# Optimization experiments

Measured on AMD Instinct MI355X. Metric: run time of the kernel, lower is better.

## Reference

```python
import jax, jax.numpy as jnp
import numpy as np

H = 1024          # hiddenSize
V = 50257         # outputSize (vocab)
L = 512           # maxLength (encoder length)


def setup_inputs() -> dict:
    key = jax.random.key(0)
    ks = jax.random.split(key, 16)
    s = 0.02
    return {
        "input": jax.random.randint(ks[0], (1,), 0, V),
        "hidden": jax.random.normal(ks[1], (1, 1, H), jnp.float32),
        "encoder_outputs": jax.random.normal(ks[2], (L, H), jnp.float32),
        "emb": jax.random.normal(ks[3], (V, H), jnp.float32) * s,
        "W_attn": jax.random.normal(ks[4], (L, 2 * H), jnp.float32) * s,
        "b_attn": jnp.zeros((L,), jnp.float32),
        "W_comb": jax.random.normal(ks[5], (H, 2 * H), jnp.float32) * s,
        "b_comb": jnp.zeros((H,), jnp.float32),
        "W_ih": jax.random.normal(ks[6], (3 * H, H), jnp.float32) * s,
        "W_hh": jax.random.normal(ks[7], (3 * H, H), jnp.float32) * s,
        "b_ih": jnp.zeros((3 * H,), jnp.float32),
        "b_hh": jnp.zeros((3 * H,), jnp.float32),
        "W_out": jax.random.normal(ks[8], (V, H), jnp.float32) * s,
        "b_out": jnp.zeros((V,), jnp.float32),
    }


def reference(input, hidden, encoder_outputs, emb, W_attn, b_attn,
              W_comb, b_comb, W_ih, W_hh, b_ih, b_hh, W_out, b_out):
    # embedding lookup: [1, H] (dropout p=0 -> identity)
    embedded = emb[input]
    h = hidden[0]                                   # [1, H]
    # attention over encoder positions
    attn_logits = jnp.concatenate([embedded, h], axis=1) @ W_attn.T + b_attn
    attn_weights = jax.nn.softmax(attn_logits, axis=1)      # [1, L]
    attn_applied = attn_weights @ encoder_outputs           # [1, H]
    # combine and relu
    x = jnp.concatenate([embedded, attn_applied], axis=1) @ W_comb.T + b_comb
    x = jax.nn.relu(x)                                      # [1, H]
    # single GRU step (PyTorch gate layout: r, z, n)
    gi = x @ W_ih.T + b_ih                                  # [1, 3H]
    gh = h @ W_hh.T + b_hh                                  # [1, 3H]
    i_r, i_z, i_n = jnp.split(gi, 3, axis=1)
    h_r, h_z, h_n = jnp.split(gh, 3, axis=1)
    r = jax.nn.sigmoid(i_r + h_r)
    z = jax.nn.sigmoid(i_z + h_z)
    n = jnp.tanh(i_n + r * h_n)
    h_new = (1.0 - z) * n + z * h                           # [1, H]
    # output distribution
    output = jax.nn.log_softmax(h_new @ W_out.T + b_out, axis=1)  # [1, V]
    return output, h_new[None], attn_weights
```

## Files before the change

### kernel.cpp

```cpp
#include <hip/hip_runtime.h>
#include <cmath>

#define H 1024
#define V 50257
#define L 512
#define NB5 1571

__device__ __forceinline__ float wred_sum(float v) {
#pragma unroll
    for (int o = 32; o > 0; o >>= 1) v += __shfl_xor(v, o, 64);
    return v;
}
__device__ __forceinline__ float wred_max(float v) {
#pragma unroll
    for (int o = 32; o > 0; o >>= 1) v = fmaxf(v, __shfl_xor(v, o, 64));
    return v;
}
__device__ __forceinline__ float dot4(float4 a, float4 b) {
    return a.x * b.x + a.y * b.y + a.z * b.z + a.w * b.w;
}
__device__ __forceinline__ void ms_merge(float& m, float& s, float m2, float s2) {
    float M = fmaxf(m, m2);
    if (M == -INFINITY) { m = M; s = 0.f; return; }
    s = s * expf(m - M) + s2 * expf(m2 - M);
    m = M;
}

__global__ void k_phase1(const int* __restrict__ tok,
                         const float* __restrict__ hid,
                         const float* __restrict__ emb,
                         const float* __restrict__ Wa,
                         const float* __restrict__ ba,
                         const float* __restrict__ Whh,
                         const float* __restrict__ bhh,
                         float* __restrict__ lg,
                         float* __restrict__ gh,
                         float* __restrict__ aa) {
    const int t = threadIdx.x;
    const int lane = t & 63, wv = t >> 6;
    if (blockIdx.x < 512) {
        const int l = blockIdx.x;
        const float4* wr = (const float4*)(Wa + (size_t)l * 2048);
        const float4* e4 = (const float4*)(emb + (size_t)tok[0] * H);
        const float4* h4 = (const float4*)hid;
        float acc = 0.f;
#pragma unroll
        for (int i = 0; i < 2; ++i) {
            int f = t + i * 256;
            float4 w = wr[f];
            float4 s = (f < 256) ? e4[f] : h4[f - 256];
            acc += dot4(w, s);
        }
        __shared__ float sm[4];
        acc = wred_sum(acc);
        if (lane == 0) sm[wv] = acc;
        __syncthreads();
        if (t == 0) lg[l] = sm[0] + sm[1] + sm[2] + sm[3] + ba[l];
    } else {
        const int j = (blockIdx.x - 512) * 4 + wv;
        const float4* wh = (const float4*)(Whh + (size_t)j * H);
        const float4* h4 = (const float4*)hid;
        float acc = 0.f;
#pragma unroll
        for (int k = 0; k < 4; ++k) {
            int f = 64 * k + lane;
            acc += dot4(wh[f], h4[f]);
        }
        acc = wred_sum(acc);
        if (lane == 0) gh[j] = acc + bhh[j];
        if (blockIdx.x == 512) {
            aa[t] = 0.f; aa[t + 256] = 0.f; aa[t + 512] = 0.f; aa[t + 768] = 0.f;
        }
    }
}

__global__ void k_attn(const float* __restrict__ lg,
                       const float* __restrict__ enc,
                       float* __restrict__ wout,
                       float* __restrict__ aa) {
    const int t = threadIdx.x;
    const int lane = t & 63, wv = t >> 6;
    __shared__ float red[4];
    __shared__ float swL[512];
    float v0 = lg[t], v1 = lg[t + 256];
    float m = wred_max(fmaxf(v0, v1));
    if (lane == 0) red[wv] = m;
    __syncthreads();
    const float M = fmaxf(fmaxf(red[0], red[1]), fmaxf(red[2], red[3]));
    float e0 = expf(v0 - M), e1 = expf(v1 - M);
    float sl = wred_sum(e0 + e1);
    __syncthreads();
    if (lane == 0) red[wv] = sl;
    __syncthreads();
    const float S = red[0] + red[1] + red[2] + red[3];
    swL[t] = e0 / S;
    swL[t + 256] = e1 / S;
    __syncthreads();
    if (blockIdx.x == 0) { wout[t] = swL[t]; wout[t + 256] = swL[t + 256]; }
    const int l0 = blockIdx.x * 16;
    float a0 = 0.f, a1 = 0.f, a2 = 0.f, a3 = 0.f;
#pragma unroll 4
    for (int l = l0; l < l0 + 16; ++l) {
        const float w = swL[l];
        const float* er = enc + (size_t)l * H;
        a0 += w * er[t];
        a1 += w * er[t + 256];
        a2 += w * er[t + 512];
        a3 += w * er[t + 768];
    }
    atomicAdd(&aa[t], a0);
    atomicAdd(&aa[t + 256], a1);
    atomicAdd(&aa[t + 512], a2);
    atomicAdd(&aa[t + 768], a3);
}

__global__ void k_comb(const int* __restrict__ tok,
                       const float* __restrict__ emb,
                       const float* __restrict__ aa,
                       const float* __restrict__ Wc,
                       const float* __restrict__ bcb,
                       float* __restrict__ xv) {
    const int lane = threadIdx.x & 63, wv = threadIdx.x >> 6;
    const int j = blockIdx.x * 4 + wv;
    const float4* wr = (const float4*)(Wc + (size_t)j * 2048);
    const float4* e4 = (const float4*)(emb + (size_t)tok[0] * H);
    const float4* a4 = (const float4*)aa;
    float acc = 0.f;
#pragma unroll
    for (int k = 0; k < 8; ++k) {
        int f = 64 * k + lane;
        float4 s = (k < 4) ? e4[f] : a4[f - 256];
        acc += dot4(wr[f], s);
    }
    acc = wred_sum(acc);
    if (lane == 0) xv[j] = fmaxf(acc + bcb[j], 0.f);
}

__global__ void k_gates_gru(const float* __restrict__ xv,
                            const float* __restrict__ hid,
                            const float* __restrict__ Wih,
                            const float* __restrict__ bih,
                            const float* __restrict__ gh,
                            float* __restrict__ hn_out,
                            float* __restrict__ hn_ws) {
    const int lane = threadIdx.x & 63, wv = threadIdx.x >> 6;
    const int j = blockIdx.x * 4 + wv;
    const float4* x4 = (const float4*)xv;
    float4 xreg[4];
#pragma unroll
    for (int k = 0; k < 4; ++k) xreg[k] = x4[64 * k + lane];
    float g[3];
#pragma unroll
    for (int p = 0; p < 3; ++p) {
        const float4* wr = (const float4*)(Wih + (size_t)(j + p * H) * H);
        float acc = 0.f;
#pragma unroll
        for (int k = 0; k < 4; ++k) acc += dot4(wr[64 * k + lane], xreg[k]);
        g[p] = wred_sum(acc) + bih[j + p * H];
    }
    if (lane == 0) {
        float r = 1.f / (1.f + expf(-(g[0] + gh[j])));
        float z = 1.f / (1.f + expf(-(g[1] + gh[j + H])));
        float n = tanhf(g[2] + r * gh[j + 2 * H]);
        float hv = (1.f - z) * n + z * hid[j];
        hn_out[j] = hv;
        hn_ws[j] = hv;
    }
}

__global__ void k_out_gemv(const float* __restrict__ hn,
                           const float* __restrict__ Wo,
                           const float* __restrict__ bo,
                           float* __restrict__ logits,
                           float* __restrict__ pm,
                           float* __restrict__ ps) {
    const int lane = threadIdx.x & 63, wv = threadIdx.x >> 6;
    const int b = blockIdx.x;
    const float4* h4 = (const float4*)hn;
    float4 hreg[4];
#pragma unroll
    for (int k = 0; k < 4; ++k) hreg[k] = h4[64 * k + lane];
    float m = -INFINITY, s = 0.f;
#pragma unroll
    for (int i = 0; i < 8; ++i) {
        const int v = b * 32 + wv * 8 + i;
        if (v < V) {
            const float4* wr = (const float4*)(Wo + (size_t)v * H);
            float acc = 0.f;
#pragma unroll
            for (int k = 0; k < 4; ++k) acc += dot4(wr[64 * k + lane], hreg[k]);
            acc = wred_sum(acc);
            const float logit = acc + bo[v];
            if (lane == 0) logits[v] = logit;
            const float M = fmaxf(m, logit);
            s = s * expf(m - M) + expf(logit - M);
            m = M;
        }
    }
    __shared__ float smm[4], sms[4];
    if (lane == 0) { smm[wv] = m; sms[wv] = s; }
    __syncthreads();
    if (threadIdx.x == 0) {
        float M = smm[0], S = sms[0];
#pragma unroll
        for (int i = 1; i < 4; ++i) ms_merge(M, S, smm[i], sms[i]);
        pm[b] = M; ps[b] = S;
    }
}

__global__ void k_finalize(float* __restrict__ out,
                           const float* __restrict__ pm,
                           const float* __restrict__ ps) {
    const int t = threadIdx.x;
    const int lane = t & 63, wv = t >> 6;
    float m = -INFINITY, s = 0.f;
    for (int i = t; i < NB5; i += 256) ms_merge(m, s, pm[i], ps[i]);
#pragma unroll
    for (int o = 32; o > 0; o >>= 1) {
        float m2 = __shfl_xor(m, o, 64);
        float s2 = __shfl_xor(s, o, 64);
        ms_merge(m, s, m2, s2);
    }
    __shared__ float smm[4], sms[4];
    __shared__ float Cs;
    if (lane == 0) { smm[wv] = m; sms[wv] = s; }
    __syncthreads();
    if (t == 0) {
        float M = smm[0], S = sms[0];
#pragma unroll
        for (int i = 1; i < 4; ++i) ms_merge(M, S, smm[i], sms[i]);
        Cs = M + logf(S);
    }
    __syncthreads();
    const float C = Cs;
    const int v = blockIdx.x * 256 + t;
    if (v < V) out[v] -= C;
}

extern "C" void kernel_launch(void* const* d_in, const int* in_sizes, int n_in,
                              void* d_out, int out_size, void* d_ws, size_t ws_size,
                              hipStream_t stream) {
    const int*   tok = (const int*)d_in[0];
    const float* hid = (const float*)d_in[1];
    const float* enc = (const float*)d_in[2];
    const float* emb = (const float*)d_in[3];
    const float* Wa  = (const float*)d_in[4];
    const float* ba  = (const float*)d_in[5];
    const float* Wc  = (const float*)d_in[6];
    const float* bc  = (const float*)d_in[7];
    const float* Wih = (const float*)d_in[8];
    const float* Whh = (const float*)d_in[9];
    const float* bih = (const float*)d_in[10];
    const float* bhh = (const float*)d_in[11];
    const float* Wo  = (const float*)d_in[12];
    const float* bo  = (const float*)d_in[13];

    float* out = (float*)d_out;
    float* ws  = (float*)d_ws;
    float* wlog = ws;
    float* aa   = ws + 512;
    float* xv   = ws + 1536;
    float* gh   = ws + 2560;
    float* hn   = ws + 5632;
    float* pm   = ws + 6656;
    float* psum = ws + 8256;

    float* out_logits = out;
    float* out_hnew   = out + V;
    float* out_attnw  = out + V + H;

    k_phase1<<<1280, 256, 0, stream>>>(tok, hid, emb, Wa, ba, Whh, bhh, wlog, gh, aa);
    k_attn<<<32, 256, 0, stream>>>(wlog, enc, out_attnw, aa);
    k_comb<<<256, 256, 0, stream>>>(tok, emb, aa, Wc, bc, xv);
    k_gates_gru<<<256, 256, 0, stream>>>(xv, hid, Wih, bih, gh, out_hnew, hn);
    k_out_gemv<<<NB5, 256, 0, stream>>>(hn, Wo, bo, out_logits, pm, psum);
    k_finalize<<<197, 256, 0, stream>>>(out_logits, pm, psum);
}
```

Measured before the change: 58.45 us.

## Fuse attention softmax and weighted sum into phase1 using unnormalized exp accumulation

Removes the separate attention kernel. Phase1 blocks now compute exp(logit) without subtracting the max, accumulate the sum and the exp-weighted encoder rows through atomics into four partial buffers, and leave the normalization to k_comb. A memset replaces the in-kernel zeroing. The out GEMV also switches from an online softmax to a two-pass max/sum over register-held logits. Skipping max subtraction risks overflow for large attention logits, and the memset adds an API call.

Measured after the change: 66.11 us. 1.13x slower.

```diff
diff --git a/kernel.cpp b/kernel.cpp
--- a/kernel.cpp
+++ b/kernel.cpp
@@ -9,11 +9,6 @@
 __device__ __forceinline__ float wred_sum(float v) {
 #pragma unroll
     for (int o = 32; o > 0; o >>= 1) v += __shfl_xor(v, o, 64);
-    return v;
-}
-__device__ __forceinline__ float wred_max(float v) {
-#pragma unroll
-    for (int o = 32; o > 0; o >>= 1) v = fmaxf(v, __shfl_xor(v, o, 64));
     return v;
 }
 __device__ __forceinline__ float dot4(float4 a, float4 b) {
@@ -31,35 +26,48 @@
                          const float* __restrict__ emb,
                          const float* __restrict__ Wa,
                          const float* __restrict__ ba,
+                         const float* __restrict__ enc,
                          const float* __restrict__ Whh,
                          const float* __restrict__ bhh,
-                         float* __restrict__ lg,
-                         float* __restrict__ gh,
-                         float* __restrict__ aa) {
+                         float* __restrict__ num4,
+                         float* __restrict__ Sacc,
+                         float* __restrict__ elg,
+                         float* __restrict__ gh) {
     const int t = threadIdx.x;
     const int lane = t & 63, wv = t >> 6;
-    if (blockIdx.x < 512) {
-        const int l = blockIdx.x;
+    const float4* h4 = (const float4*)hid;
+    if (blockIdx.x < 128) {
+        const int l = blockIdx.x * 4 + wv;
+        const float4* e4 = (const float4*)(emb + (size_t)tok[0] * H);
         const float4* wr = (const float4*)(Wa + (size_t)l * 2048);
-        const float4* e4 = (const float4*)(emb + (size_t)tok[0] * H);
-        const float4* h4 = (const float4*)hid;
         float acc = 0.f;
 #pragma unroll
-        for (int i = 0; i < 2; ++i) {
-            int f = t + i * 256;
-            float4 w = wr[f];
+        for (int k = 0; k < 8; ++k) {
+            int f = 64 * k + lane;
             float4 s = (f < 256) ? e4[f] : h4[f - 256];
-            acc += dot4(w, s);
-        }
-        __shared__ float sm[4];
+            acc += dot4(wr[f], s);
+        }
         acc = wred_sum(acc);
-        if (lane == 0) sm[wv] = acc;
+        const float e = expf(acc + ba[l]);
+        __shared__ float se[4];
+        if (lane == 0) { se[wv] = e; elg[l] = e; }
         __syncthreads();
-        if (t == 0) lg[l] = sm[0] + sm[1] + sm[2] + sm[3] + ba[l];
+        if (t == 0) atomicAdd(Sacc, se[0] + se[1] + se[2] + se[3]);
+        float4 a = make_float4(0.f, 0.f, 0.f, 0.f);
+#pragma unroll
+        for (int r = 0; r < 4; ++r) {
+            const float w = se[r];
+            const float4 v = ((const float4*)(enc + (size_t)(blockIdx.x * 4 + r) * H))[t];
+            a.x += w * v.x; a.y += w * v.y; a.z += w * v.z; a.w += w * v.w;
+        }
+        float* dst = num4 + (size_t)(blockIdx.x & 3) * 1024 + 4 * t;
+        atomicAdd(dst + 0, a.x);
+        atomicAdd(dst + 1, a.y);
+        atomicAdd(dst + 2, a.z);
+        atomicAdd(dst + 3, a.w);
     } else {
-        const int j = (blockIdx.x - 512) * 4 + wv;
+        const int j = (blockIdx.x - 128) * 4 + wv;
         const float4* wh = (const float4*)(Whh + (size_t)j * H);
-        const float4* h4 = (const float4*)hid;
         float acc = 0.f;
 #pragma unroll
         for (int k = 0; k < 4; ++k) {
@@ -68,72 +76,43 @@
         }
         acc = wred_sum(acc);
         if (lane == 0) gh[j] = acc + bhh[j];
-        if (blockIdx.x == 512) {
-            aa[t] = 0.f; aa[t + 256] = 0.f; aa[t + 512] = 0.f; aa[t + 768] = 0.f;
-        }
-    }
-}
-
-__global__ void k_attn(const float* __restrict__ lg,
-                       const float* __restrict__ enc,
-                       float* __restrict__ wout,
-                       float* __restrict__ aa) {
+    }
+}
+
+__global__ void k_comb(const int* __restrict__ tok,
+                       const float* __restrict__ emb,
+                       const float* __restrict__ num4,
+                       const float* __restrict__ Sacc,
+                       const float* __restrict__ elg,
+                       const float* __restrict__ Wc,
+                       const float* __restrict__ bcb,
+                       float* __restrict__ xv,
+                       float* __restrict__ wout) {
     const int t = threadIdx.x;
     const int lane = t & 63, wv = t >> 6;
-    __shared__ float red[4];
-    __shared__ float swL[512];
-    float v0 = lg[t], v1 = lg[t + 256];
-    float m = wred_max(fmaxf(v0, v1));
-    if (lane == 0) red[wv] = m;
-    __syncthreads();
-    const float M = fmaxf(fmaxf(red[0], red[1]), fmaxf(red[2], red[3]));
-    float e0 = expf(v0 - M), e1 = expf(v1 - M);
-    float sl = wred_sum(e0 + e1);
-    __syncthreads();
-    if (lane == 0) red[wv] = sl;
-    __syncthreads();
-    const float S = red[0] + red[1] + red[2] + red[3];
-    swL[t] = e0 / S;
-    swL[t + 256] = e1 / S;
-    __syncthreads();
-    if (blockIdx.x == 0) { wout[t] = swL[t]; wout[t + 256] = swL[t + 256]; }
-    const int l0 = blockIdx.x * 16;
-    float a0 = 0.f, a1 = 0.f, a2 = 0.f, a3 = 0.f;
-#pragma unroll 4
-    for (int l = l0; l < l0 + 16; ++l) {
-        const float w = swL[l];
-        const float* er = enc + (size_t)l * H;
-        a0 += w * er[t];
-        a1 += w * er[t + 256];
-        a2 += w * er[t + 512];
-        a3 += w * er[t + 768];
-    }
-    atomicAdd(&aa[t], a0);
-    atomicAdd(&aa[t + 256], a1);
-    atomicAdd(&aa[t + 512], a2);
-    atomicAdd(&aa[t + 768], a3);
-}
-
-__global__ void k_comb(const int* __restrict__ tok,
-                       const float* __restrict__ emb,
-                       const float* __restrict__ aa,
-                       const float* __restrict__ Wc,
-                       const float* __restrict__ bcb,
-                       float* __restrict__ xv) {
-    const int lane = threadIdx.x & 63, wv = threadIdx.x >> 6;
     const int j = blockIdx.x * 4 + wv;
+    const float invS = 1.f / Sacc[0];
+    const float4* e4 = (const float4*)(emb + (size_t)tok[0] * H);
+    const float4* n4 = (const float4*)num4;
     const float4* wr = (const float4*)(Wc + (size_t)j * 2048);
-    const float4* e4 = (const float4*)(emb + (size_t)tok[0] * H);
-    const float4* a4 = (const float4*)aa;
     float acc = 0.f;
 #pragma unroll
-    for (int k = 0; k < 8; ++k) {
+    for (int k = 0; k < 4; ++k) {
         int f = 64 * k + lane;
-        float4 s = (k < 4) ? e4[f] : a4[f - 256];
-        acc += dot4(wr[f], s);
+        acc += dot4(wr[f], e4[f]);
+        float4 s0 = n4[f], s1 = n4[256 + f], s2 = n4[512 + f], s3 = n4[768 + f];
+        float4 aa = make_float4((s0.x + s1.x + s2.x + s3.x) * invS,
+                                (s0.y + s1.y + s2.y + s3.y) * invS,
+                                (s0.z + s1.z + s2.z + s3.z) * invS,
+                                (s0.w + s1.w + s2.w + s3.w) * invS);
+        acc += dot4(wr[256 + f], aa);
     }
     acc = wred_sum(acc);
     if (lane == 0) xv[j] = fmaxf(acc + bcb[j], 0.f);
+    if (blockIdx.x == 0) {
+        wout[t] = elg[t] * invS;
+        wout[t + 256] = elg[t + 256] * invS;
+    }
 }
 
 __global__ void k_gates_gru(const float* __restrict__ xv,
@@ -180,7 +159,8 @@
     float4 hreg[4];
 #pragma unroll
     for (int k = 0; k < 4; ++k) hreg[k] = h4[64 * k + lane];
-    float m = -INFINITY, s = 0.f;
+    float lv[8];
+    int nvalid = 0;
 #pragma unroll
     for (int i = 0; i < 8; ++i) {
         const int v = b * 32 + wv * 8 + i;
@@ -189,14 +169,14 @@
             float acc = 0.f;
 #pragma unroll
             for (int k = 0; k < 4; ++k) acc += dot4(wr[64 * k + lane], hreg[k]);
-            acc = wred_sum(acc);
-            const float logit = acc + bo[v];
-            if (lane == 0) logits[v] = logit;
-            const float M = fmaxf(m, logit);
-            s = s * expf(m - M) + expf(logit - M);
-            m = M;
-        }
-    }
+            acc = wred_sum(acc) + bo[v];
+            if (lane == 0) logits[v] = acc;
+            lv[nvalid++] = acc;
+        }
+    }
+    float m = -INFINITY, s = 0.f;
+    for (int i = 0; i < nvalid; ++i) m = fmaxf(m, lv[i]);
+    for (int i = 0; i < nvalid; ++i) s += expf(lv[i] - m);
     __shared__ float smm[4], sms[4];
     if (lane == 0) { smm[wv] = m; sms[wv] = s; }
     __syncthreads();
@@ -257,21 +237,23 @@
 
     float* out = (float*)d_out;
     float* ws  = (float*)d_ws;
-    float* wlog = ws;
-    float* aa   = ws + 512;
-    float* xv   = ws + 1536;
-    float* gh   = ws + 2560;
-    float* hn   = ws + 5632;
-    float* pm   = ws + 6656;
-    float* psum = ws + 8256;
+    float* num4 = ws;
+    float* Sacc = ws + 4096;
+    float* elg  = ws + 4112;
+    float* gh   = ws + 4624;
+    float* xv   = ws + 7696;
+    float* hn   = ws + 8720;
+    float* pm   = ws + 9744;
+    float* psum = ws + 11316;
 
     float* out_logits = out;
     float* out_hnew   = out + V;
     float* out_attnw  = out + V + H;
 
-    k_phase1<<<1280, 256, 0, stream>>>(tok, hid, emb, Wa, ba, Whh, bhh, wlog, gh, aa);
-    k_attn<<<32, 256, 0, stream>>>(wlog, enc, out_attnw, aa);
-    k_comb<<<256, 256, 0, stream>>>(tok, emb, aa, Wc, bc, xv);
+    hipMemsetAsync(ws, 0, 4097 * sizeof(float), stream);
+    k_phase1<<<896, 256, 0, stream>>>(tok, hid, emb, Wa, ba, enc, Whh, bhh,
+                                      num4, Sacc, elg, gh);
+    k_comb<<<256, 256, 0, stream>>>(tok, emb, num4, Sacc, elg, Wc, bc, xv, out_attnw);
     k_gates_gru<<<256, 256, 0, stream>>>(xv, hid, Wih, bih, gh, out_hnew, hn);
     k_out_gemv<<<NB5, 256, 0, stream>>>(hn, Wo, bo, out_logits, pm, psum);
     k_finalize<<<197, 256, 0, stream>>>(out_logits, pm, psum);
```
